# Kernel optimization log

Measured on AMD Instinct MI355X. Metric: run time of the kernel, lower is better.

The kernel has to match this reference:

```python
import jax, jax.numpy as jnp
import numpy as np

L = 8          # number of QTT cores = log2(init_reso)
RESO = 256     # init_reso
MAX_RANK = 256
N_SAMPLES = 4096


def _qtt_ranks(L, max_rank):
    return [min(8 ** k, 8 ** (L - k), max_rank) for k in range(L + 1)]


def setup_inputs() -> dict:
    key = jax.random.key(0)
    ranks = _qtt_ranks(L, MAX_RANK)
    keys = jax.random.split(key, L + 1)
    inp = {}
    for l in range(L):
        shape = (ranks[l], 8, ranks[l + 1])
        scale = (shape[0] * shape[1]) ** -0.5  # keep chain products O(1)
        inp[f"core{l}"] = jax.random.normal(keys[l], shape, dtype=jnp.float32) * scale
    inp["coords_xyz"] = jax.random.randint(keys[L], (N_SAMPLES, 3), 0, RESO)
    return inp


def _coords_to_qtt(coords_xyz, num_cores):
    # coords_xyz: (N, 3) int. Per core l (most-significant bit first):
    # c_l = 4*bit_x + 2*bit_y + bit_z in [0, 8)  -> shape (L, N)
    x, y, z = coords_xyz[:, 0], coords_xyz[:, 1], coords_xyz[:, 2]
    shifts = jnp.arange(num_cores - 1, -1, -1)[:, None]  # (L, 1)
    bx = (x[None, :] >> shifts) & 1
    by = (y[None, :] >> shifts) & 1
    bz = (z[None, :] >> shifts) & 1
    return 4 * bx + 2 * by + bz


def _sample_tt(cores, coords):
    # cores[l]: (r_l, 8, r_{l+1}); coords: (L, N)
    # v starts as first core slice: (N, r_1)  (r_0 == 1)
    v = cores[0][0, coords[0], :]
    for l in range(1, len(cores)):
        # gathered slice: (r_l, N, r_{l+1}) -> (N, r_l, r_{l+1})
        g = jnp.transpose(cores[l][:, coords[l], :], (1, 0, 2))
        v = jnp.einsum('nr,nrs->ns', v, g)
    return v[:, 0]  # r_L == 1 -> (N,)


def reference(core0, core1, core2, core3, core4, core5, core6, core7, coords_xyz):
    cores = [core0, core1, core2, core3, core4, core5, core6, core7]
    coords = _coords_to_qtt(coords_xyz, len(cores))
    return _sample_tt(cores, coords)
```

## Files before the change

kernel.cpp:

```cpp
#include <hip/hip_runtime.h>


typedef unsigned int u32;

__device__ __forceinline__ void fma4(float4& c, float a, const float4& b) {
    c.x = fmaf(a, b.x, c.x); c.y = fmaf(a, b.y, c.y);
    c.z = fmaf(a, b.z, c.z); c.w = fmaf(a, b.w, c.w);
}
__device__ __forceinline__ int digit_of(int x, int y, int z, int sh) {
    return 4*((x>>sh)&1) + 2*((y>>sh)&1) + ((z>>sh)&1);
}

__global__ __launch_bounds__(256, 4) void prep_kernel(
    const float* __restrict__ C4, float* __restrict__ C4t)
{
    const int t = threadIdx.x;
    const int cb = blockIdx.x;
    const int d4 = cb >> 2, s5q = cb & 3;
#pragma unroll 8
    for (int j = 0; j < 64; ++j) {
        const int s5 = s5q*64 + j;
        C4t[(size_t)d4*65536 + (size_t)s5*256 + t] =
            C4[(size_t)t*2048 + d4*256 + s5];
    }
}

__device__ __forceinline__ void kgemm4(
    const float* __restrict__ Bg, int rowStride,
    const float (*As)[260], int r0, int ln,
    float4& acc0, float4& acc1, float4& acc2, float4& acc3)
{
    const float* gp = Bg + ln * 4;
    float4 bA0 = *(const float4*)(gp + (size_t)0*rowStride);
    float4 bA1 = *(const float4*)(gp + (size_t)1*rowStride);
    float4 bA2 = *(const float4*)(gp + (size_t)2*rowStride);
    float4 bA3 = *(const float4*)(gp + (size_t)3*rowStride);
    float4 bB0 = *(const float4*)(gp + (size_t)4*rowStride);
    float4 bB1 = *(const float4*)(gp + (size_t)5*rowStride);
    float4 bB2 = *(const float4*)(gp + (size_t)6*rowStride);
    float4 bB3 = *(const float4*)(gp + (size_t)7*rowStride);

#define QTT_COMP(b0, b1, b2, b3, kb)                                   \
    {   const float4 a0 = *(const float4*)&As[r0+0][(kb)];             \
        const float4 a1 = *(const float4*)&As[r0+1][(kb)];             \
        const float4 a2 = *(const float4*)&As[r0+2][(kb)];             \
        const float4 a3 = *(const float4*)&As[r0+3][(kb)];             \
        fma4(acc0, a0.x, b0); fma4(acc0, a0.y, b1);                    \
        fma4(acc0, a0.z, b2); fma4(acc0, a0.w, b3);                    \
        fma4(acc1, a1.x, b0); fma4(acc1, a1.y, b1);                    \
        fma4(acc1, a1.z, b2); fma4(acc1, a1.w, b3);                    \
        fma4(acc2, a2.x, b0); fma4(acc2, a2.y, b1);                    \
        fma4(acc2, a2.z, b2); fma4(acc2, a2.w, b3);                    \
        fma4(acc3, a3.x, b0); fma4(acc3, a3.y, b1);                    \
        fma4(acc3, a3.z, b2); fma4(acc3, a3.w, b3); }

#pragma unroll 1
    for (int s = 0; s < 32; ++s) {
        const int k0 = s * 8;
        QTT_COMP(bA0, bA1, bA2, bA3, k0);
        if (s < 31) {
            bA0 = *(const float4*)(gp + (size_t)(k0+ 8)*rowStride);
            bA1 = *(const float4*)(gp + (size_t)(k0+ 9)*rowStride);
            bA2 = *(const float4*)(gp + (size_t)(k0+10)*rowStride);
            bA3 = *(const float4*)(gp + (size_t)(k0+11)*rowStride);
        }
        QTT_COMP(bB0, bB1, bB2, bB3, k0 + 4);
        if (s < 31) {
            bB0 = *(const float4*)(gp + (size_t)(k0+12)*rowStride);
            bB1 = *(const float4*)(gp + (size_t)(k0+13)*rowStride);
            bB2 = *(const float4*)(gp + (size_t)(k0+14)*rowStride);
            bB3 = *(const float4*)(gp + (size_t)(k0+15)*rowStride);
        }
    }
#undef QTT_COMP
}

__global__ __launch_bounds__(256, 2) void tables_kernel(
    const float* __restrict__ C0, const float* __restrict__ C1,
    const float* __restrict__ C2, const float* __restrict__ C3,
    const float* __restrict__ C4t, const float* __restrict__ C5,
    const float* __restrict__ C6, const float* __restrict__ C7,
    float* __restrict__ P3, float* __restrict__ U)
{
    __shared__ __align__(16) struct {
        float small[4][4][64];
        float As[16][260];
    } u;
    const int t = threadIdx.x;
    const int ln = t & 63, wv = t >> 6;
    const int bx = blockIdx.x;

    float4 acc0 = make_float4(0,0,0,0), acc1 = make_float4(0,0,0,0);
    float4 acc2 = make_float4(0,0,0,0), acc3 = make_float4(0,0,0,0);

    if (bx < 256) {
        const int d3 = bx & 7, d2p = (bx >> 3) & 3, d0 = bx >> 5;

        const int d1base = (wv & 1) * 4;
#pragma unroll
        for (int i = 0; i < 4; ++i) {
            float acc = 0.f;
#pragma unroll
            for (int r8 = 0; r8 < 8; ++r8)
                acc = fmaf(C0[d0*8 + r8],
                           C1[r8*512 + (d1base + i)*64 + ln], acc);
            u.small[wv][i][ln] = acc;
        }
        __syncthreads();

        const int d2 = d2p*2 + (wv >> 1);
        {
            float4 a0 = make_float4(0,0,0,0), a1 = make_float4(0,0,0,0);
            float4 a2 = make_float4(0,0,0,0), a3 = make_float4(0,0,0,0);
            const float* c2base = C2 + d2*256 + ln*4;
#pragma unroll
            for (int j4 = 0; j4 < 16; ++j4) {
                const float4 v0 = *(const float4*)&u.small[wv][0][j4*4];
                const float4 v1 = *(const float4*)&u.small[wv][1][j4*4];
                const float4 v2 = *(const float4*)&u.small[wv][2][j4*4];
                const float4 v3 = *(const float4*)&u.small[wv][3][j4*4];
#define QTT_ASTEP(jj, comp)                                            \
                { const float4 c2 = *(const float4*)(c2base +          \
                      (size_t)(j4*4 + jj)*2048);                       \
                  fma4(a0, v0.comp, c2); fma4(a1, v1.comp, c2);        \
                  fma4(a2, v2.comp, c2); fma4(a3, v3.comp, c2); }
                QTT_ASTEP(0, x) QTT_ASTEP(1, y) QTT_ASTEP(2, z) QTT_ASTEP(3, w)
#undef QTT_ASTEP
            }
            *(float4*)&u.As[wv*4+0][ln*4] = a0;
            *(float4*)&u.As[wv*4+1][ln*4] = a1;
            *(float4*)&u.As[wv*4+2][ln*4] = a2;
            *(float4*)&u.As[wv*4+3][ln*4] = a3;
        }
        __syncthreads();

        kgemm4(C3 + d3*256, 2048, u.As, wv*4, ln, acc0, acc1, acc2, acc3);

        const int rb = d0*512 + d2*8 + d3;
        *(float4*)(P3 + (size_t)(rb + (d1base+0)*64)*256 + ln*4) = acc0;
        *(float4*)(P3 + (size_t)(rb + (d1base+1)*64)*256 + ln*4) = acc1;
        *(float4*)(P3 + (size_t)(rb + (d1base+2)*64)*256 + ln*4) = acc2;
        *(float4*)(P3 + (size_t)(rb + (d1base+3)*64)*256 + ln*4) = acc3;
    } else {
        const int ub = bx - 256;
        const int qtile = ub & 31, d4 = ub >> 5;
        const int d5 = qtile >> 2;

        float4 creg[16];
#pragma unroll
        for (int j4 = 0; j4 < 16; ++j4)
            creg[j4] = *(const float4*)(C5 + (size_t)t*512 + d5*64 + j4*4);

#pragma unroll
        for (int i = 0; i < 4; ++i) {
            const int r = wv*4 + i;
            const int d6 = (qtile & 3)*2 + (r >> 3), d7 = r & 7;
            float acc = 0.f;
#pragma unroll
            for (int jj = 0; jj < 8; ++jj)
                acc = fmaf(C6[ln*64 + d6*8 + jj], C7[jj*8 + d7], acc);
            u.small[wv][i][ln] = acc;
        }
        __syncthreads();

#pragma unroll 1
        for (int r = 0; r < 16; ++r) {
            float acc = 0.f;
#pragma unroll
            for (int j4 = 0; j4 < 16; ++j4) {
                const float4 s6 = *(const float4*)&u.small[r >> 2][r & 3][j4*4];
                const float4 c5 = creg[j4];
                acc = fmaf(c5.x, s6.x, acc); acc = fmaf(c5.y, s6.y, acc);
                acc = fmaf(c5.z, s6.z, acc); acc = fmaf(c5.w, s6.w, acc);
            }
            u.As[r][t] = acc;
        }
        __syncthreads();

        kgemm4(C4t + (size_t)d4*65536, 256, u.As, wv*4, ln,
               acc0, acc1, acc2, acc3);

        const int rb = d4*512 + qtile*16 + wv*4;
        *(float4*)(U + (size_t)(rb + 0)*256 + ln*4) = acc0;
        *(float4*)(U + (size_t)(rb + 1)*256 + ln*4) = acc1;
        *(float4*)(U + (size_t)(rb + 2)*256 + ln*4) = acc2;
        *(float4*)(U + (size_t)(rb + 3)*256 + ln*4) = acc3;
    }
}

__global__ __launch_bounds__(256) void final_kernel(
    const float* __restrict__ P3, const float* __restrict__ U,
    const int* __restrict__ coords, int n, float* __restrict__ out)
{
    const int ln = threadIdx.x & 63, wv = threadIdx.x >> 6;
    const int s0 = blockIdx.x * 8 + wv * 2;

    float p[2] = {0.f, 0.f};
    int valid[2];
#pragma unroll
    for (int i = 0; i < 2; ++i) {
        const int s = s0 + i;
        valid[i] = (s < n);
        if (valid[i]) {
            const int x = coords[3*s], y = coords[3*s+1], z = coords[3*s+2];
            const int a  = digit_of(x,y,z,7)*512 + digit_of(x,y,z,6)*64
                         + digit_of(x,y,z,5)*8  + digit_of(x,y,z,4);
            const int d4 = digit_of(x,y,z,3);
            const int q  = digit_of(x,y,z,2)*64 + digit_of(x,y,z,1)*8
                         + digit_of(x,y,z,0);
            const float4 p4 = *(const float4*)(P3 + (size_t)a*256 + ln*4);
            const float4 u4 = *(const float4*)(U + (size_t)(d4*512 + q)*256 + ln*4);
            p[i] = fmaf(p4.x, u4.x, fmaf(p4.y, u4.y,
                   fmaf(p4.z, u4.z, p4.w * u4.w)));
        }
    }
#pragma unroll
    for (int m = 1; m <= 32; m <<= 1) {
        p[0] += __shfl_xor(p[0], m);
        p[1] += __shfl_xor(p[1], m);
    }
    if (ln == 0) {
        if (valid[0]) out[s0]     = p[0];
        if (valid[1]) out[s0 + 1] = p[1];
    }
}

extern "C" void kernel_launch(void* const* d_in, const int* in_sizes, int n_in,
                              void* d_out, int out_size, void* d_ws, size_t ws_size,
                              hipStream_t stream) {
    const float* C0 = (const float*)d_in[0];
    const float* C1 = (const float*)d_in[1];
    const float* C2 = (const float*)d_in[2];
    const float* C3 = (const float*)d_in[3];
    const float* C4 = (const float*)d_in[4];
    const float* C5 = (const float*)d_in[5];
    const float* C6 = (const float*)d_in[6];
    const float* C7 = (const float*)d_in[7];
    const int* coords = (const int*)d_in[8];
    float* out = (float*)d_out;

    const int n = in_sizes[8] / 3;

    float* P3  = (float*)d_ws;
    float* U   = P3 + 4096*256;
    float* C4t = U  + 4096*256;

    prep_kernel<<<32, 256, 0, stream>>>(C4, C4t);
    tables_kernel<<<512, 256, 0, stream>>>(
        C0, C1, C2, C3, C4t, C5, C6, C7, P3, U);
    final_kernel<<<(n + 7) / 8, 256, 0, stream>>>(P3, U, coords, n, out);
}
```

Measured before the change: 115.9 us.

## Split table GEMM K across waves with LDS reduction and double block count

The table-building kernel now gives each block 8 output rows instead of 16 and launches twice as many blocks. Each wave takes a quarter of the K dimension (64 of 256) for all 8 rows, and the partial sums are combined through a shared-memory reduction. Occupancy is raised to 4 blocks per SM via launch bounds and a smaller shared-memory union. The goal is more parallelism and latency hiding in the GEMM phase. The cost is redundant prologue work per block, extra barriers and the reduction step.

```diff
diff --git a/kernel.cpp b/kernel.cpp
--- a/kernel.cpp
+++ b/kernel.cpp
@@ -25,12 +25,24 @@
     }
 }
 
-__device__ __forceinline__ void kgemm4(
+__device__ __forceinline__ void comp8(
+    const float (*As)[260], int kk,
+    const float4& b0, const float4& b1, const float4& b2, const float4& b3,
+    float4* acc)
+{
+#pragma unroll
+    for (int r = 0; r < 8; ++r) {
+        const float4 a = *(const float4*)&As[r][kk];
+        fma4(acc[r], a.x, b0); fma4(acc[r], a.y, b1);
+        fma4(acc[r], a.z, b2); fma4(acc[r], a.w, b3);
+    }
+}
+
+__device__ __forceinline__ void kgemm8(
     const float* __restrict__ Bg, int rowStride,
-    const float (*As)[260], int r0, int ln,
-    float4& acc0, float4& acc1, float4& acc2, float4& acc3)
-{
-    const float* gp = Bg + ln * 4;
+    const float (*As)[260], int kbase, int ln, float4* acc)
+{
+    const float* gp = Bg + (size_t)kbase * rowStride + (size_t)ln * 4;
     float4 bA0 = *(const float4*)(gp + (size_t)0*rowStride);
     float4 bA1 = *(const float4*)(gp + (size_t)1*rowStride);
     float4 bA2 = *(const float4*)(gp + (size_t)2*rowStride);
@@ -40,151 +52,144 @@
     float4 bB2 = *(const float4*)(gp + (size_t)6*rowStride);
     float4 bB3 = *(const float4*)(gp + (size_t)7*rowStride);
 
-#define QTT_COMP(b0, b1, b2, b3, kb)                                   \
-    {   const float4 a0 = *(const float4*)&As[r0+0][(kb)];             \
-        const float4 a1 = *(const float4*)&As[r0+1][(kb)];             \
-        const float4 a2 = *(const float4*)&As[r0+2][(kb)];             \
-        const float4 a3 = *(const float4*)&As[r0+3][(kb)];             \
-        fma4(acc0, a0.x, b0); fma4(acc0, a0.y, b1);                    \
-        fma4(acc0, a0.z, b2); fma4(acc0, a0.w, b3);                    \
-        fma4(acc1, a1.x, b0); fma4(acc1, a1.y, b1);                    \
-        fma4(acc1, a1.z, b2); fma4(acc1, a1.w, b3);                    \
-        fma4(acc2, a2.x, b0); fma4(acc2, a2.y, b1);                    \
-        fma4(acc2, a2.z, b2); fma4(acc2, a2.w, b3);                    \
-        fma4(acc3, a3.x, b0); fma4(acc3, a3.y, b1);                    \
-        fma4(acc3, a3.z, b2); fma4(acc3, a3.w, b3); }
-
 #pragma unroll 1
-    for (int s = 0; s < 32; ++s) {
+    for (int s = 0; s < 8; ++s) {
         const int k0 = s * 8;
-        QTT_COMP(bA0, bA1, bA2, bA3, k0);
-        if (s < 31) {
+        comp8(As, kbase + k0, bA0, bA1, bA2, bA3, acc);
+        if (s < 7) {
             bA0 = *(const float4*)(gp + (size_t)(k0+ 8)*rowStride);
             bA1 = *(const float4*)(gp + (size_t)(k0+ 9)*rowStride);
             bA2 = *(const float4*)(gp + (size_t)(k0+10)*rowStride);
             bA3 = *(const float4*)(gp + (size_t)(k0+11)*rowStride);
         }
-        QTT_COMP(bB0, bB1, bB2, bB3, k0 + 4);
-        if (s < 31) {
+        comp8(As, kbase + k0 + 4, bB0, bB1, bB2, bB3, acc);
+        if (s < 7) {
             bB0 = *(const float4*)(gp + (size_t)(k0+12)*rowStride);
             bB1 = *(const float4*)(gp + (size_t)(k0+13)*rowStride);
             bB2 = *(const float4*)(gp + (size_t)(k0+14)*rowStride);
             bB3 = *(const float4*)(gp + (size_t)(k0+15)*rowStride);
         }
     }
-#undef QTT_COMP
-}
-
-__global__ __launch_bounds__(256, 2) void tables_kernel(
+}
+
+__global__ __launch_bounds__(256, 4) void tables_kernel(
     const float* __restrict__ C0, const float* __restrict__ C1,
     const float* __restrict__ C2, const float* __restrict__ C3,
     const float* __restrict__ C4t, const float* __restrict__ C5,
     const float* __restrict__ C6, const float* __restrict__ C7,
     float* __restrict__ P3, float* __restrict__ U)
 {
-    __shared__ __align__(16) struct {
-        float small[4][4][64];
-        float As[16][260];
+    __shared__ __align__(16) union {
+        struct { float small[8][64]; float As[8][260]; } g;
+        float red[4][4][256];
     } u;
     const int t = threadIdx.x;
     const int ln = t & 63, wv = t >> 6;
     const int bx = blockIdx.x;
 
-    float4 acc0 = make_float4(0,0,0,0), acc1 = make_float4(0,0,0,0);
-    float4 acc2 = make_float4(0,0,0,0), acc3 = make_float4(0,0,0,0);
-
-    if (bx < 256) {
-        const int d3 = bx & 7, d2p = (bx >> 3) & 3, d0 = bx >> 5;
-
-        const int d1base = (wv & 1) * 4;
-#pragma unroll
-        for (int i = 0; i < 4; ++i) {
-            float acc = 0.f;
+    float4 acc[8];
+#pragma unroll
+    for (int r = 0; r < 8; ++r) acc[r] = make_float4(0,0,0,0);
+
+    const float* Bg;
+    int rowStride, rowBase, rowStep;
+    float* outP;
+
+    if (bx < 512) {
+        const int d3 = bx & 7, d2 = (bx >> 3) & 7, d0 = bx >> 6;
+
+#pragma unroll
+        for (int j = 0; j < 2; ++j) {
+            const int idx = t + 256*j, d1 = idx >> 6, c = idx & 63;
+            float a = 0.f;
 #pragma unroll
             for (int r8 = 0; r8 < 8; ++r8)
-                acc = fmaf(C0[d0*8 + r8],
-                           C1[r8*512 + (d1base + i)*64 + ln], acc);
-            u.small[wv][i][ln] = acc;
-        }
-        __syncthreads();
-
-        const int d2 = d2p*2 + (wv >> 1);
+                a = fmaf(C0[d0*8 + r8], C1[r8*512 + d1*64 + c], a);
+            u.g.small[d1][c] = a;
+        }
+        __syncthreads();
+
         {
             float4 a0 = make_float4(0,0,0,0), a1 = make_float4(0,0,0,0);
-            float4 a2 = make_float4(0,0,0,0), a3 = make_float4(0,0,0,0);
             const float* c2base = C2 + d2*256 + ln*4;
+#pragma unroll 8
+            for (int j = 0; j < 64; ++j) {
+                const float4 c2 = *(const float4*)(c2base + (size_t)j*2048);
+                fma4(a0, u.g.small[wv*2 + 0][j], c2);
+                fma4(a1, u.g.small[wv*2 + 1][j], c2);
+            }
+            *(float4*)&u.g.As[wv*2 + 0][ln*4] = a0;
+            *(float4*)&u.g.As[wv*2 + 1][ln*4] = a1;
+        }
+        __syncthreads();
+
+        Bg = C3 + d3*256; rowStride = 2048;
+        rowBase = d0*512 + d2*8 + d3; rowStep = 64;
+        outP = P3;
+    } else {
+        const int ub = bx - 512;
+        const int qt = ub & 63, d4 = ub >> 6;
+        const int d5 = qt >> 3, d6 = qt & 7;
+
+#pragma unroll
+        for (int j = 0; j < 2; ++j) {
+            const int idx = t + 256*j, r = idx >> 6, s6 = idx & 63;
+            float a = 0.f;
+#pragma unroll
+            for (int jj = 0; jj < 8; ++jj)
+                a = fmaf(C6[s6*64 + d6*8 + jj], C7[jj*8 + r], a);
+            u.g.small[r][s6] = a;
+        }
+        __syncthreads();
+
+        {
+            float accT[8];
+#pragma unroll
+            for (int r = 0; r < 8; ++r) accT[r] = 0.f;
 #pragma unroll
             for (int j4 = 0; j4 < 16; ++j4) {
-                const float4 v0 = *(const float4*)&u.small[wv][0][j4*4];
-                const float4 v1 = *(const float4*)&u.small[wv][1][j4*4];
-                const float4 v2 = *(const float4*)&u.small[wv][2][j4*4];
-                const float4 v3 = *(const float4*)&u.small[wv][3][j4*4];
-#define QTT_ASTEP(jj, comp)                                            \
-                { const float4 c2 = *(const float4*)(c2base +          \
-                      (size_t)(j4*4 + jj)*2048);                       \
-                  fma4(a0, v0.comp, c2); fma4(a1, v1.comp, c2);        \
-                  fma4(a2, v2.comp, c2); fma4(a3, v3.comp, c2); }
-                QTT_ASTEP(0, x) QTT_ASTEP(1, y) QTT_ASTEP(2, z) QTT_ASTEP(3, w)
-#undef QTT_ASTEP
+                const float4 c5 = *(const float4*)(C5 + (size_t)t*512
+                                                   + d5*64 + j4*4);
+#pragma unroll
+                for (int r = 0; r < 8; ++r) {
+                    const float4 s6v = *(const float4*)&u.g.small[r][j4*4];
+                    accT[r] = fmaf(c5.x, s6v.x, accT[r]);
+                    accT[r] = fmaf(c5.y, s6v.y, accT[r]);
+                    accT[r] = fmaf(c5.z, s6v.z, accT[r]);
+                    accT[r] = fmaf(c5.w, s6v.w, accT[r]);
+                }
             }
-            *(float4*)&u.As[wv*4+0][ln*4] = a0;
-            *(float4*)&u.As[wv*4+1][ln*4] = a1;
-            *(float4*)&u.As[wv*4+2][ln*4] = a2;
-            *(float4*)&u.As[wv*4+3][ln*4] = a3;
-        }
-        __syncthreads();
-
-        kgemm4(C3 + d3*256, 2048, u.As, wv*4, ln, acc0, acc1, acc2, acc3);
-
-        const int rb = d0*512 + d2*8 + d3;
-        *(float4*)(P3 + (size_t)(rb + (d1base+0)*64)*256 + ln*4) = acc0;
-        *(float4*)(P3 + (size_t)(rb + (d1base+1)*64)*256 + ln*4) = acc1;
-        *(float4*)(P3 + (size_t)(rb + (d1base+2)*64)*256 + ln*4) = acc2;
-        *(float4*)(P3 + (size_t)(rb + (d1base+3)*64)*256 + ln*4) = acc3;
-    } else {
-        const int ub = bx - 256;
-        const int qtile = ub & 31, d4 = ub >> 5;
-        const int d5 = qtile >> 2;
-
-        float4 creg[16];
-#pragma unroll
-        for (int j4 = 0; j4 < 16; ++j4)
-            creg[j4] = *(const float4*)(C5 + (size_t)t*512 + d5*64 + j4*4);
-
-#pragma unroll
-        for (int i = 0; i < 4; ++i) {
-            const int r = wv*4 + i;
-            const int d6 = (qtile & 3)*2 + (r >> 3), d7 = r & 7;
-            float acc = 0.f;
-#pragma unroll
-            for (int jj = 0; jj < 8; ++jj)
-                acc = fmaf(C6[ln*64 + d6*8 + jj], C7[jj*8 + d7], acc);
-            u.small[wv][i][ln] = acc;
-        }
-        __syncthreads();
-
-#pragma unroll 1
-        for (int r = 0; r < 16; ++r) {
-            float acc = 0.f;
-#pragma unroll
-            for (int j4 = 0; j4 < 16; ++j4) {
-                const float4 s6 = *(const float4*)&u.small[r >> 2][r & 3][j4*4];
-                const float4 c5 = creg[j4];
-                acc = fmaf(c5.x, s6.x, acc); acc = fmaf(c5.y, s6.y, acc);
-                acc = fmaf(c5.z, s6.z, acc); acc = fmaf(c5.w, s6.w, acc);
-            }
-            u.As[r][t] = acc;
-        }
-        __syncthreads();
-
-        kgemm4(C4t + (size_t)d4*65536, 256, u.As, wv*4, ln,
-               acc0, acc1, acc2, acc3);
-
-        const int rb = d4*512 + qtile*16 + wv*4;
-        *(float4*)(U + (size_t)(rb + 0)*256 + ln*4) = acc0;
-        *(float4*)(U + (size_t)(rb + 1)*256 + ln*4) = acc1;
-        *(float4*)(U + (size_t)(rb + 2)*256 + ln*4) = acc2;
-        *(float4*)(U + (size_t)(rb + 3)*256 + ln*4) = acc3;
+#pragma unroll
+            for (int r = 0; r < 8; ++r) u.g.As[r][t] = accT[r];
+        }
+        __syncthreads();
+
+        Bg = C4t + (size_t)d4*65536; rowStride = 256;
+        rowBase = d4*512 + qt*8; rowStep = 1;
+        outP = U;
+    }
+
+    kgemm8(Bg, rowStride, u.g.As, wv*64, ln, acc);
+
+    __syncthreads();
+
+#pragma unroll
+    for (int ph = 0; ph < 2; ++ph) {
+#pragma unroll
+        for (int i = 0; i < 4; ++i)
+            *(float4*)&u.red[wv][i][ln*4] = acc[ph*4 + i];
+        __syncthreads();
+        {
+            float4 v        = *(const float4*)&u.red[0][wv][ln*4];
+            const float4 p1 = *(const float4*)&u.red[1][wv][ln*4];
+            const float4 p2 = *(const float4*)&u.red[2][wv][ln*4];
+            const float4 p3 = *(const float4*)&u.red[3][wv][ln*4];
+            v.x += p1.x + p2.x + p3.x; v.y += p1.y + p2.y + p3.y;
+            v.z += p1.z + p2.z + p3.z; v.w += p1.w + p2.w + p3.w;
+            const int r = ph*4 + wv;
+            *(float4*)(outP + (size_t)(rowBase + rowStep*r)*256 + ln*4) = v;
+        }
+        __syncthreads();
     }
 }
 
@@ -246,7 +251,7 @@
     float* C4t = U  + 4096*256;
 
     prep_kernel<<<32, 256, 0, stream>>>(C4, C4t);
-    tables_kernel<<<512, 256, 0, stream>>>(
+    tables_kernel<<<1024, 256, 0, stream>>>(
         C0, C1, C2, C3, C4t, C5, C6, C7, P3, U);
     final_kernel<<<(n + 7) / 8, 256, 0, stream>>>(P3, U, coords, n, out);
 }
```

Result: slower. 144.6 us (+24.8%).
